# Kernel optimization log

Hardware: AMD Instinct MI355X
Metric: run time of the kernel (lower is better)

## Reference

```python
import jax, jax.numpy as jnp
import numpy as np

DIM = 1024
N_HEADS = 16
HEAD_DIM = DIM // N_HEADS
B, T = 2, 2048


def setup_inputs() -> dict:
    key = jax.random.key(0)
    ks = jax.random.split(key, 6)
    x = jax.random.normal(ks[0], (B, T, DIM), dtype=jnp.float32)
    # causal 0/1 mask, broadcastable over batch and heads
    mask = jnp.tril(jnp.ones((T, T), dtype=jnp.int32))[None, None, :, :]
    s = 1.0 / np.sqrt(DIM)
    W_qkv = jax.random.normal(ks[1], (DIM, 3 * DIM), dtype=jnp.float32) * s
    b_qkv = jnp.zeros((3 * DIM,), dtype=jnp.float32)
    W_proj = jax.random.normal(ks[2], (DIM, DIM), dtype=jnp.float32) * s
    b_proj = jnp.zeros((DIM,), dtype=jnp.float32)
    return {"x": x, "W_qkv": W_qkv, "b_qkv": b_qkv, "W_proj": W_proj, "b_proj": b_proj, "mask": mask}


def reference(x, W_qkv, b_qkv, W_proj, b_proj, mask):
    Bx, Tx, C = x.shape
    qkv = x @ W_qkv + b_qkv  # [B,T,3C]
    q, k, v = jnp.split(qkv, 3, axis=-1)
    # [B,T,C] -> [B,H,T,Dh]
    def split_heads(t):
        return t.reshape(Bx, Tx, N_HEADS, HEAD_DIM).transpose(0, 2, 1, 3)
    q, k, v = split_heads(q), split_heads(k), split_heads(v)
    att = jnp.einsum('bhqd,bhkd->bhqk', q, k) / jnp.sqrt(jnp.float32(HEAD_DIM))
    att = jnp.where(mask == 0, jnp.float32(-jnp.inf), att)
    att = jax.nn.softmax(att, axis=-1)
    # dropout is identity in eval mode
    out = jnp.einsum('bhqk,bhkd->bhqd', att, v)
    out = out.transpose(0, 2, 1, 3).reshape(Bx, Tx, C)
    return out @ W_proj + b_proj
```

## Files before the change

kernel.cpp:

```cpp
#include <hip/hip_runtime.h>
#include <hip/hip_bf16.h>
#include <stdint.h>

#define DIM   1024
#define NHEAD 16
#define HD    64
#define SEQ   2048
#define NTOK  4096
#define QKV_REGION (NTOK * DIM)

typedef short          bf16x8 __attribute__((ext_vector_type(8)));
typedef float          f32x4  __attribute__((ext_vector_type(4)));
typedef float          f32x16 __attribute__((ext_vector_type(16)));
typedef unsigned short u16x8  __attribute__((ext_vector_type(8)));
typedef unsigned short u16x4  __attribute__((ext_vector_type(4)));

__device__ __forceinline__ unsigned short f2bf(float f) {
  union { float f; unsigned u; } x; x.f = f;
  unsigned r = x.u + 0x7FFFu + ((x.u >> 16) & 1u);
  return (unsigned short)(r >> 16);
}

__device__ __forceinline__ unsigned pack2bf_tr(float a, float b) {
  union { float f; unsigned u; } x, y; x.f = a; y.f = b;
  return (x.u >> 16) | (y.u & 0xFFFF0000u);
}

__device__ __forceinline__ void gld16(void* lds, const void* g) {
  __builtin_amdgcn_global_load_lds(
      (const __attribute__((address_space(1))) unsigned int*)g,
      (__attribute__((address_space(3))) unsigned int*)lds, 16, 0, 0);
}

__global__ __launch_bounds__(256) void k_prep(const float* __restrict__ x,
                                              unsigned short* __restrict__ xb,
                                              const float* __restrict__ Wqkv,
                                              unsigned short* __restrict__ wqkvt,
                                              const float* __restrict__ Wproj,
                                              unsigned short* __restrict__ wprojt) {
  __shared__ unsigned short t[64][72];
  const int bid = blockIdx.x, tid = threadIdx.x;
  if (bid < 2048) {
    size_t i = ((size_t)bid * 256 + tid) * 8;
    float4 a = *(const float4*)(x + i);
    float4 b = *(const float4*)(x + i + 4);
    u16x8 o;
    o[0] = f2bf(a.x); o[1] = f2bf(a.y); o[2] = f2bf(a.z); o[3] = f2bf(a.w);
    o[4] = f2bf(b.x); o[5] = f2bf(b.y); o[6] = f2bf(b.z); o[7] = f2bf(b.w);
    *(u16x8*)(xb + i) = o;
    return;
  }
  const float* in; unsigned short* out; int C, bx, by;
  if (bid < 2816) { in = Wqkv; out = wqkvt; C = 3072; bx = (bid - 2048) % 48; by = (bid - 2048) / 48; }
  else            { in = Wproj; out = wprojt; C = 1024; bx = (bid - 2816) % 16; by = (bid - 2816) / 16; }
  const int R = 1024;
  int r0 = by * 64, c0 = bx * 64;
  int rr = tid >> 4, cc = (tid & 15) * 4;
#pragma unroll
  for (int p = 0; p < 4; p++) {
    int r = p * 16 + rr;
    float4 v = *(const float4*)(in + (size_t)(r0 + r) * C + c0 + cc);
    t[r][cc + 0] = f2bf(v.x); t[r][cc + 1] = f2bf(v.y);
    t[r][cc + 2] = f2bf(v.z); t[r][cc + 3] = f2bf(v.w);
  }
  __syncthreads();
#pragma unroll
  for (int p = 0; p < 4; p++) {
    int c = p * 16 + rr;
    u16x4 v;
    v[0] = t[cc + 0][c]; v[1] = t[cc + 1][c];
    v[2] = t[cc + 2][c]; v[3] = t[cc + 3][c];
    *(u16x4*)(out + (size_t)(c0 + c) * R + r0 + cc) = v;
  }
}

__global__ __launch_bounds__(256) void k_tr_v(const unsigned short* __restrict__ v,
                                              unsigned short* __restrict__ vt) {
  __shared__ unsigned short s[64][72];
  int bh = blockIdx.y, t0 = blockIdx.x * 64;
  const unsigned short* in = v + (size_t)bh * SEQ * HD + (size_t)t0 * HD;
  unsigned short* out = vt + (size_t)bh * HD * SEQ + t0;
  int tid = threadIdx.x;
  int rr = tid >> 3, cc = (tid & 7) * 8;
#pragma unroll
  for (int p = 0; p < 2; p++) {
    int r = p * 32 + rr;
    u16x8 x = *(const u16x8*)(in + r * HD + cc);
#pragma unroll
    for (int j = 0; j < 8; j++) s[r][cc + j] = x[j];
  }
  __syncthreads();
#pragma unroll
  for (int p = 0; p < 2; p++) {
    int d = p * 32 + rr;
    u16x8 o;
#pragma unroll
    for (int j = 0; j < 8; j++) o[j] = s[cc + j][d];
    *(u16x8*)(out + (size_t)d * SEQ + cc) = o;
  }
}

template <int EPI>
__global__ __launch_bounds__(256) void k_gemm_bt(const unsigned short* __restrict__ A,
                                                 const unsigned short* __restrict__ Bt,
                                                 const float* __restrict__ bias,
                                                 void* __restrict__ Cout,
                                                 int M, int N, int K) {
  __shared__ unsigned short Al[128 * 64];
  __shared__ unsigned short Bl[128 * 64];
  const int tid = threadIdx.x, lane = tid & 63, w = tid >> 6;
  const int wm = w >> 1, wn = w & 1;
  const int m0 = blockIdx.y * 128, n0 = blockIdx.x * 128;
  const int l31 = lane & 31, hl = lane >> 5;

  f32x16 acc[2][2];
#pragma unroll
  for (int mt = 0; mt < 2; mt++)
#pragma unroll
    for (int nt = 0; nt < 2; nt++)
#pragma unroll
      for (int r = 0; r < 16; r++) acc[mt][nt][r] = 0.f;

  for (int k0 = 0; k0 < K; k0 += 64) {
    __syncthreads();
#pragma unroll
    for (int i = 0; i < 4; i++) {
      int row = w * 32 + i * 8 + (lane >> 3);
      int ch = (lane & 7) ^ (row & 7);
      gld16(&Al[(w * 32 + i * 8) * 64], A + (size_t)(m0 + row) * K + k0 + ch * 8);
      gld16(&Bl[(w * 32 + i * 8) * 64], Bt + (size_t)(n0 + row) * K + k0 + ch * 8);
    }
    __syncthreads();
#pragma unroll
    for (int ks = 0; ks < 4; ks++) {
      bf16x8 af[2], bfr[2];
#pragma unroll
      for (int mt = 0; mt < 2; mt++) {
        int row = wm * 64 + mt * 32 + l31;
        int ch = (2 * ks + hl) ^ (row & 7);
        af[mt] = *(const bf16x8*)&Al[row * 64 + ch * 8];
      }
#pragma unroll
      for (int nt = 0; nt < 2; nt++) {
        int row = wn * 64 + nt * 32 + l31;
        int ch = (2 * ks + hl) ^ (row & 7);
        bfr[nt] = *(const bf16x8*)&Bl[row * 64 + ch * 8];
      }
#pragma unroll
      for (int mt = 0; mt < 2; mt++)
#pragma unroll
        for (int nt = 0; nt < 2; nt++)
          acc[mt][nt] = __builtin_amdgcn_mfma_f32_32x32x16_bf16(af[mt], bfr[nt], acc[mt][nt], 0, 0, 0);
    }
  }

#pragma unroll
  for (int mt = 0; mt < 2; mt++) {
#pragma unroll
    for (int nt = 0; nt < 2; nt++) {
      int col = n0 + wn * 64 + nt * 32 + l31;
      float bv = bias[col];
#pragma unroll
      for (int rg = 0; rg < 4; rg++)
#pragma unroll
        for (int ri = 0; ri < 4; ri++) {
          int row = m0 + wm * 64 + mt * 32 + ri + rg * 8 + hl * 4;
          float val = acc[mt][nt][rg * 4 + ri] + bv;
          if (EPI == 1) {
            ((float*)Cout)[(size_t)row * N + col] = val;
          } else {
            unsigned short* dst = (unsigned short*)Cout;
            int reg = col >> 10, nn = col & 1023;
            if (reg == 0) val *= 0.18033688011112042f;
            int h = nn >> 6, d = nn & 63;
            int b = row >> 11, t = row & 2047;
            size_t idx = (size_t)reg * QKV_REGION +
                         ((size_t)(b * NHEAD + h) * SEQ + t) * HD + d;
            dst[idx] = f2bf(val);
          }
        }
    }
  }
}

__global__ __launch_bounds__(512, 4) void k_attn(const unsigned short* __restrict__ Q,
                                                 const unsigned short* __restrict__ K,
                                                 const unsigned short* __restrict__ Vt,
                                                 unsigned short* __restrict__ O) {
  __shared__ unsigned short kl[2][2][64 * 64];
  __shared__ unsigned short vl[2][2][64 * 64];
  __shared__ float ml2[128];
  const int tid = threadIdx.x, lane = tid & 63, w = tid >> 6;
  const int hl = lane >> 5, q32 = lane & 31;
  const bool hb = (hl != 0);
  const int h = w >> 2, wr = w & 3;
  const int id = blockIdx.x;
  const int bh = id & 31;
  const int qt = (id < 256) ? (15 - (id >> 5)) : ((id >> 5) - 8);
  const unsigned short* Qb = Q + (size_t)bh * SEQ * HD;
  const unsigned short* Kb = K + (size_t)bh * SEQ * HD;
  const unsigned short* Vb = Vt + (size_t)bh * HD * SEQ;

  const int wq = qt * 128 + wr * 32;
  const int qmax = wq + 31;
  const int qg = wq + q32;
  const int nlo = qt + 1;
  const int kt0 = h ? nlo : 0;

  bf16x8 qf[4];
  {
    const unsigned short* qp = Qb + (size_t)(wq + q32) * HD + hl * 8;
#pragma unroll
    for (int ks = 0; ks < 4; ks++) qf[ks] = *(const bf16x8*)(qp + ks * 16);
  }

  f32x16 oacc[2];
#pragma unroll
  for (int nd = 0; nd < 2; nd++)
#pragma unroll
    for (int r = 0; r < 16; r++) oacc[nd][r] = 0.f;
  float lpart = 0.f;

#define ASTAGE(S, BUF)                                                                   \
  if ((S) < nlo) {                                                                       \
    const int kb_ = (kt0 + (S)) * 64;                                                    \
    _Pragma("unroll")                                                                    \
    for (int i = 0; i < 2; i++) {                                                        \
      int row = wr * 16 + i * 8 + (lane >> 3);                                           \
      int ch = (lane & 7) ^ (row & 7);                                                   \
      gld16(&kl[h][BUF][(wr * 16 + i * 8) * 64], Kb + (size_t)(kb_ + row) * HD + ch * 8);\
      gld16(&vl[h][BUF][(wr * 16 + i * 8) * 64], Vb + (size_t)row * SEQ + kb_ + ch * 8); \
    }                                                                                    \
  }

  ASTAGE(0, 0);
  __syncthreads();
  int cur = 0;

  for (int s = 0; s < nlo; s++) {
    ASTAGE(s + 1, cur ^ 1);
    const int kb = (kt0 + s) * 64;
    if (kb <= qmax) {
      f32x16 sacc[2];
#pragma unroll
      for (int nk = 0; nk < 2; nk++)
#pragma unroll
        for (int r = 0; r < 16; r++) sacc[nk][r] = 0.f;
      __builtin_amdgcn_s_setprio(1);
#pragma unroll
      for (int ks = 0; ks < 4; ks++) {
#pragma unroll
        for (int nk = 0; nk < 2; nk++) {
          int krow = nk * 32 + q32;
          int ch = (2 * ks + hl) ^ (krow & 7);
          bf16x8 kf = *(const bf16x8*)&kl[h][cur][krow * 64 + ch * 8];
          sacc[nk] = __builtin_amdgcn_mfma_f32_32x32x16_bf16(kf, qf[ks], sacc[nk], 0, 0, 0);
        }
      }
      __builtin_amdgcn_s_setprio(0);

      const bool nm = (kb + 63 > wq);
      if (nm) {
        const int kvbase = kb + hl * 4;
#pragma unroll
        for (int nk = 0; nk < 2; nk++)
#pragma unroll
          for (int rg = 0; rg < 4; rg++)
#pragma unroll
            for (int ri = 0; ri < 4; ri++) {
              int kv = kvbase + nk * 32 + rg * 8 + ri;
              if (kv > qg) sacc[nk][rg * 4 + ri] = -__builtin_inff();
            }
      }

#pragma unroll
      for (int nk = 0; nk < 2; nk++) {
#pragma unroll
        for (int r = 0; r < 16; r++)
          sacc[nk][r] = __builtin_amdgcn_exp2f(sacc[nk][r]);
        __builtin_amdgcn_sched_barrier(0);
      }
      {
        float ts[8];
#pragma unroll
        for (int i = 0; i < 8; i++)
          ts[i] = (sacc[0][i] + sacc[0][i + 8]) + (sacc[1][i] + sacc[1][i + 8]);
#pragma unroll
        for (int i = 0; i < 4; i++) ts[i] = ts[i] + ts[i + 4];
        lpart += (ts[0] + ts[2]) + (ts[1] + ts[3]);
      }

#pragma unroll
      for (int nk = 0; nk < 2; nk++) {
        unsigned cc[4][2];
#pragma unroll
        for (int m = 0; m < 4; m++) {
          cc[m][0] = pack2bf_tr(sacc[nk][4 * m + 0], sacc[nk][4 * m + 1]);
          cc[m][1] = pack2bf_tr(sacc[nk][4 * m + 2], sacc[nk][4 * m + 3]);
        }
        unsigned rv[2][2];
#pragma unroll
        for (int mm = 0; mm < 2; mm++) {
          unsigned sx = hb ? cc[2 * mm][0] : cc[2 * mm + 1][0];
          unsigned sy = hb ? cc[2 * mm][1] : cc[2 * mm + 1][1];
          rv[mm][0] = (unsigned)__shfl_xor((int)sx, 32);
          rv[mm][1] = (unsigned)__shfl_xor((int)sy, 32);
        }
        __builtin_amdgcn_s_setprio(1);
#pragma unroll
        for (int sl = 0; sl < 2; sl++) {
          const int me = 2 * sl;
          union { bf16x8 v; unsigned u[4]; } Afr;
          Afr.u[0] = hb ? rv[sl][0] : cc[me][0];
          Afr.u[1] = hb ? rv[sl][1] : cc[me][1];
          Afr.u[2] = hb ? cc[me + 1][0] : rv[sl][0];
          Afr.u[3] = hb ? cc[me + 1][1] : rv[sl][1];
          const int ss = nk * 2 + sl;
#pragma unroll
          for (int nd = 0; nd < 2; nd++) {
            int vrow = nd * 32 + q32;
            int ch = (2 * ss + hl) ^ (vrow & 7);
            bf16x8 vf = *(const bf16x8*)&vl[h][cur][vrow * 64 + ch * 8];
            oacc[nd] = __builtin_amdgcn_mfma_f32_32x32x16_bf16(Afr.v, vf, oacc[nd], 0, 0, 0);
          }
        }
        __builtin_amdgcn_s_setprio(0);
      }
    }
    __syncthreads();
    cur ^= 1;
  }
#undef ASTAGE

  float lf = lpart + __shfl_xor(lpart, 32);
  float* o1 = (float*)&kl[0][0][0];
  if (h == 1) {
#pragma unroll
    for (int nd = 0; nd < 2; nd++)
#pragma unroll
      for (int rg = 0; rg < 4; rg++)
#pragma unroll
        for (int ri = 0; ri < 4; ri++) {
          int row = wr * 32 + ri + rg * 8 + hl * 4;
          o1[row * 64 + nd * 32 + q32] = oacc[nd][rg * 4 + ri];
        }
    if (lane < 32) ml2[wr * 32 + lane] = lf;
  }
  __syncthreads();
  if (h == 0) {
    const int b = bh >> 4, hh = bh & 15;
    float l1 = ml2[wr * 32 + q32];
    float ainv = 1.f / (lf + l1);
#pragma unroll
    for (int rg = 0; rg < 4; rg++)
#pragma unroll
      for (int ri = 0; ri < 4; ri++) {
        int srcl = ri + rg * 8 + hl * 4;
        float bv = __shfl(ainv, srcl);
        int row = wr * 32 + srcl;
        int t = qt * 128 + row;
#pragma unroll
        for (int nd = 0; nd < 2; nd++) {
          int d = nd * 32 + q32;
          float val = (oacc[nd][rg * 4 + ri] + o1[row * 64 + d]) * bv;
          O[((size_t)(b * SEQ + t)) * DIM + hh * HD + d] = f2bf(val);
        }
      }
  }
}

extern "C" void kernel_launch(void* const* d_in, const int* in_sizes, int n_in,
                              void* d_out, int out_size, void* d_ws, size_t ws_size,
                              hipStream_t stream) {
  const float* x     = (const float*)d_in[0];
  const float* Wqkv  = (const float*)d_in[1];
  const float* bqkv  = (const float*)d_in[2];
  const float* Wproj = (const float*)d_in[3];
  const float* bproj = (const float*)d_in[4];
  float* out = (float*)d_out;

  unsigned short* ws     = (unsigned short*)d_ws;
  unsigned short* xb_vt  = ws;
  unsigned short* wqkvt  = xb_vt + 4194304;
  unsigned short* wprojt = wqkvt + 3145728;
  unsigned short* q      = wprojt + 1048576;
  unsigned short* k      = q + 4194304;
  unsigned short* v_o    = k + 4194304;

  k_prep<<<3072, 256, 0, stream>>>(x, xb_vt, Wqkv, wqkvt, Wproj, wprojt);
  k_gemm_bt<0><<<dim3(24, 32), 256, 0, stream>>>(xb_vt, wqkvt, bqkv, q, NTOK, 3072, DIM);
  k_tr_v<<<dim3(32, 32), 256, 0, stream>>>(v_o, xb_vt);
  k_attn<<<dim3(512), 512, 0, stream>>>(q, k, xb_vt, v_o);
  k_gemm_bt<1><<<dim3(8, 32), 256, 0, stream>>>(v_o, wprojt, bproj, out, NTOK, DIM, DIM);
}
```

Measured before the change: 108.3 us.

## Pipeline GEMM K-loop with triple-buffered LDS and vmcnt-gated async loads

Replaces the single-buffer, two-barrier GEMM K-loop (BK=64) with a three-stage ring of BK=32 LDS tiles. Global-to-LDS loads for stage s+2 are issued while stage s is being computed, and s_waitcnt vmcnt replaces the pre-load barrier. The swizzle is adapted to 32-wide rows, and s_setprio is raised around the MFMA block. This aims to hide global load latency behind MFMA work, at the cost of more barriers per unit of K and a dependence on exact vmcnt counts.

```diff
diff --git a/kernel.cpp b/kernel.cpp
--- a/kernel.cpp
+++ b/kernel.cpp
@@ -106,12 +106,15 @@
                                                  const float* __restrict__ bias,
                                                  void* __restrict__ Cout,
                                                  int M, int N, int K) {
-  __shared__ unsigned short Al[128 * 64];
-  __shared__ unsigned short Bl[128 * 64];
+  __shared__ unsigned short Al[3][128 * 32];
+  __shared__ unsigned short Bl[3][128 * 32];
   const int tid = threadIdx.x, lane = tid & 63, w = tid >> 6;
   const int wm = w >> 1, wn = w & 1;
   const int m0 = blockIdx.y * 128, n0 = blockIdx.x * 128;
   const int l31 = lane & 31, hl = lane >> 5;
+  const int NS = K >> 5;
+  const int srow = tid >> 2;
+  const int csw = (tid & 3) ^ ((tid >> 3) & 3);
 
   f32x16 acc[2][2];
 #pragma unroll
@@ -121,38 +124,54 @@
 #pragma unroll
       for (int r = 0; r < 16; r++) acc[mt][nt][r] = 0.f;
 
-  for (int k0 = 0; k0 < K; k0 += 64) {
-    __syncthreads();
-#pragma unroll
-    for (int i = 0; i < 4; i++) {
-      int row = w * 32 + i * 8 + (lane >> 3);
-      int ch = (lane & 7) ^ (row & 7);
-      gld16(&Al[(w * 32 + i * 8) * 64], A + (size_t)(m0 + row) * K + k0 + ch * 8);
-      gld16(&Bl[(w * 32 + i * 8) * 64], Bt + (size_t)(n0 + row) * K + k0 + ch * 8);
-    }
-    __syncthreads();
-#pragma unroll
-    for (int ks = 0; ks < 4; ks++) {
+#define GSTAGE(S)                                                                   \
+  if ((S) < NS) {                                                                   \
+    const int kk = (S) << 5;                                                        \
+    unsigned short* a_ = &Al[(S) % 3][0];                                           \
+    unsigned short* b_ = &Bl[(S) % 3][0];                                           \
+    _Pragma("unroll")                                                               \
+    for (int p = 0; p < 2; p++) {                                                   \
+      int row = p * 64 + srow;                                                      \
+      gld16(a_ + row * 32 + (tid & 3) * 8, A + (size_t)(m0 + row) * K + kk + csw * 8); \
+      gld16(b_ + row * 32 + (tid & 3) * 8, Bt + (size_t)(n0 + row) * K + kk + csw * 8);\
+    }                                                                               \
+  }
+
+  GSTAGE(0);
+  GSTAGE(1);
+  for (int s = 0; s < NS; s++) {
+    if (s < NS - 1) asm volatile("s_waitcnt vmcnt(4)" ::: "memory");
+    else            asm volatile("s_waitcnt vmcnt(0)" ::: "memory");
+    __builtin_amdgcn_s_barrier();
+    __builtin_amdgcn_sched_barrier(0);
+    const unsigned short* a_ = &Al[s % 3][0];
+    const unsigned short* b_ = &Bl[s % 3][0];
+#pragma unroll
+    for (int ks = 0; ks < 2; ks++) {
       bf16x8 af[2], bfr[2];
 #pragma unroll
       for (int mt = 0; mt < 2; mt++) {
         int row = wm * 64 + mt * 32 + l31;
-        int ch = (2 * ks + hl) ^ (row & 7);
-        af[mt] = *(const bf16x8*)&Al[row * 64 + ch * 8];
+        int ch = (ks * 2 + hl) ^ ((row >> 1) & 3);
+        af[mt] = *(const bf16x8*)&a_[row * 32 + ch * 8];
       }
 #pragma unroll
       for (int nt = 0; nt < 2; nt++) {
         int row = wn * 64 + nt * 32 + l31;
-        int ch = (2 * ks + hl) ^ (row & 7);
-        bfr[nt] = *(const bf16x8*)&Bl[row * 64 + ch * 8];
-      }
+        int ch = (ks * 2 + hl) ^ ((row >> 1) & 3);
+        bfr[nt] = *(const bf16x8*)&b_[row * 32 + ch * 8];
+      }
+      __builtin_amdgcn_s_setprio(1);
 #pragma unroll
       for (int mt = 0; mt < 2; mt++)
 #pragma unroll
         for (int nt = 0; nt < 2; nt++)
           acc[mt][nt] = __builtin_amdgcn_mfma_f32_32x32x16_bf16(af[mt], bfr[nt], acc[mt][nt], 0, 0, 0);
+      __builtin_amdgcn_s_setprio(0);
     }
-  }
+    GSTAGE(s + 2);
+  }
+#undef GSTAGE
 
 #pragma unroll
   for (int mt = 0; mt < 2; mt++) {
```

New measurement: 113.7 us. 4.9% more time.
